# Kernel tuning notes

Hardware: AMD Instinct MI355X
Metric: run time of the kernel (lower is better)

The kernel has to match this reference:

```python
import jax, jax.numpy as jnp
from jax import lax
import numpy as np

B, L, D = 8, 2048, 512
Q, K = 8, 2048


def setup_inputs() -> dict:
    key = jax.random.key(0)
    kx, kc = jax.random.split(key)
    x = jax.random.normal(kx, (B, L, D), dtype=jnp.float32)
    codebooks = jax.random.normal(kc, (Q, K, D), dtype=jnp.float32)  # Q stacked [K, D] embedding tables
    return {"x": x, "codebooks": codebooks}


def reference(x, codebooks):
    # Residual VQ: at each level, nearest-codeword lookup on the residual.
    # cdist argmin == squared-distance argmin: ||r||^2 - 2 r.c + ||c||^2.
    cb_sq = jnp.sum(codebooks * codebooks, axis=-1)  # [Q, K]

    def step(residual, level):
        cb, cb2 = level  # [K, D], [K]
        r2 = jnp.sum(residual * residual, axis=-1, keepdims=True)  # [B, L, 1]
        dots = jnp.einsum('bld,kd->blk', residual, cb)  # [B, L, K]
        dist2 = r2 - 2.0 * dots + cb2  # [B, L, K]
        idx = jnp.argmin(dist2, axis=-1)  # [B, L]
        quant = cb[idx]  # [B, L, D] gather
        return residual - quant, (idx, quant)

    _, (indices, quants) = lax.scan(step, x, (codebooks, cb_sq))
    quantized = jnp.sum(quants, axis=0)  # [B, L, D]
    indices = jnp.moveaxis(indices, 0, 1)  # [B, Q, L] (torch.stack(dim=1))
    return indices, quantized
```

## Files before the change

### kernel.cpp

```cpp
#include <hip/hip_runtime.h>

#define BB 8
#define LL 2048
#define DD 512
#define QQ 8
#define KK 2048
#define MM (BB*LL)

#define NTILES 16

typedef __attribute__((ext_vector_type(8))) short short8;
typedef __attribute__((ext_vector_type(4))) float f32x4;

#define GLDS(src, dst) __builtin_amdgcn_global_load_lds( \
    (const __attribute__((address_space(1))) void*)(src), \
    (__attribute__((address_space(3))) void*)(dst), 16, 0, 0)

#define BARX()  asm volatile("s_barrier" ::: "memory")
#define WAIT0() asm volatile("s_waitcnt vmcnt(0)" ::: "memory")

__device__ __forceinline__ ushort f2bf(float f) {
    uint u = __float_as_uint(f);
    u += 0x7FFFu + ((u >> 16) & 1u);
    return (ushort)(u >> 16);
}

__global__ __launch_bounds__(256) void cb2_kernel(const float* __restrict__ cb,
                                                  float* __restrict__ cb2) {
    int row  = blockIdx.x * 4 + (threadIdx.x >> 6);
    int lane = threadIdx.x & 63;
    const float* r = cb + (size_t)row * DD + lane * 8;
    float4 a = *(const float4*)r;
    float4 b = *(const float4*)(r + 4);
    float s = a.x*a.x + a.y*a.y + a.z*a.z + a.w*a.w
            + b.x*b.x + b.y*b.y + b.z*b.z + b.w*b.w;
    #pragma unroll
    for (int off = 32; off >= 1; off >>= 1) s += __shfl_xor(s, off);
    if (lane == 0) cb2[row] = s;
}

__global__ __launch_bounds__(256) void bprep_kernel(const float* __restrict__ cbq,
                                                    short8* __restrict__ bh2) {
    const int wid  = threadIdx.x >> 6;
    const int lane = threadIdx.x & 63;
    const int col  = blockIdx.x * 4 + wid;
    const float* src = cbq + (size_t)col * DD + lane * 8;
    float4 v0 = *(const float4*)src;
    float4 v1 = *(const float4*)(src + 4);
    short8 h;
    h[0] = (short)f2bf(v0.x); h[1] = (short)f2bf(v0.y);
    h[2] = (short)f2bf(v0.z); h[3] = (short)f2bf(v0.w);
    h[4] = (short)f2bf(v1.x); h[5] = (short)f2bf(v1.y);
    h[6] = (short)f2bf(v1.z); h[7] = (short)f2bf(v1.w);
    bh2[(size_t)col * 64 + lane] = h;
}

__global__ __launch_bounds__(256) void aprep0_kernel(const float* __restrict__ x,
                                                     float* __restrict__ resid,
                                                     short8* __restrict__ ah) {
    const int wid  = threadIdx.x >> 6;
    const int lane = threadIdx.x & 63;
    const int row  = blockIdx.x * 4 + wid;
    const float* src = x + (size_t)row * DD + lane * 8;
    float4 v0 = *(const float4*)src;
    float4 v1 = *(const float4*)(src + 4);
    float* dst = resid + (size_t)row * DD + lane * 8;
    *(float4*)dst       = v0;
    *(float4*)(dst + 4) = v1;
    short8 h;
    h[0] = (short)f2bf(v0.x); h[1] = (short)f2bf(v0.y);
    h[2] = (short)f2bf(v0.z); h[3] = (short)f2bf(v0.w);
    h[4] = (short)f2bf(v1.x); h[5] = (short)f2bf(v1.y);
    h[6] = (short)f2bf(v1.z); h[7] = (short)f2bf(v1.w);
    ah[(size_t)row * 64 + lane] = h;
}

__global__ __launch_bounds__(512, 2) void gemm_argmin_kernel(
    const short8* __restrict__ ah,
    const short8* __restrict__ bh2,
    const float*  __restrict__ cb2q,
    float*        __restrict__ blockv1,
    uint4*        __restrict__ blockmask,
    float W)
{
    __shared__ char smemc[131072];

    const int id  = blockIdx.x;
    const int xcd = id & 7;
    const int s   = id >> 3;
    const int nt  = s & 7;
    const int mt  = xcd * 8 + (s >> 3);

    const int tid  = threadIdx.x;
    const int wid  = tid >> 6;
    const int lane = tid & 63;
    const int wr   = wid >> 2;
    const int wcn  = wid & 3;
    const int l15  = lane & 15, l4 = lane >> 4;

    f32x4 acc[4][8];
    #pragma unroll
    for (int n = 0; n < 4; n++)
        #pragma unroll
        for (int m = 0; m < 8; m++) acc[n][m] = (f32x4){0.f, 0.f, 0.f, 0.f};

    const char* aSrc = (const char*)ah  + ((size_t)mt << 18);
    const char* bSrc = (const char*)bh2 + ((size_t)nt << 18);

    #define STAGEQ(tt, bufn, p) do { \
        int g_ = (p) * 512 + tid; \
        int rL_ = g_ >> 3, st_ = g_ & 7; \
        int k_ = st_ ^ (rL_ & 7); \
        char* db_ = smemc + (bufn) * 65536 + ((p) * 512 + wid * 64) * 16; \
        GLDS(aSrc + (size_t)rL_ * 1024 + (tt) * 128 + k_ * 16, db_); \
        GLDS(bSrc + (size_t)rL_ * 1024 + (tt) * 128 + k_ * 16, db_ + 32768); \
    } while (0)

    short8 af[4][2], bf[4][2];

    #define LDA(mh) do { \
        _Pragma("unroll") for (int mm = 0; mm < 4; mm++) \
        _Pragma("unroll") for (int ks = 0; ks < 2; ks++) { \
            int rL_ = wr * 128 + ((mh) * 4 + mm) * 16 + l15; \
            int c_ = ks * 4 + l4; \
            af[mm][ks] = *(const short8*)(smemc + ab + rL_ * 128 + ((c_ ^ (rL_ & 7)) << 4)); \
        } } while (0)

    #define LDB(nh) do { \
        _Pragma("unroll") for (int nn = 0; nn < 2; nn++) \
        _Pragma("unroll") for (int ks = 0; ks < 2; ks++) { \
            int cL_ = wcn * 64 + ((nh) * 2 + nn) * 16 + l15; \
            int c_ = ks * 4 + l4; \
            bf[(nh)*2+nn][ks] = *(const short8*)(smemc + ab + 32768 + cL_ * 128 + ((c_ ^ (cL_ & 7)) << 4)); \
        } } while (0)

    #define PH(mh, nh) do { \
        __builtin_amdgcn_s_setprio(1); \
        _Pragma("unroll") for (int nn = 0; nn < 2; nn++) \
        _Pragma("unroll") for (int mm = 0; mm < 4; mm++) \
        _Pragma("unroll") for (int ks = 0; ks < 2; ks++) \
            acc[(nh)*2+nn][(mh)*4+mm] = __builtin_amdgcn_mfma_f32_16x16x32_bf16( \
                bf[(nh)*2+nn][ks], af[mm][ks], acc[(nh)*2+nn][(mh)*4+mm], 0, 0, 0); \
        __builtin_amdgcn_s_setprio(0); \
    } while (0)

    STAGEQ(0, 0, 0); STAGEQ(0, 0, 1); STAGEQ(0, 0, 2); STAGEQ(0, 0, 3);
    WAIT0();
    BARX();

    for (int t = 0; t < 8; t++) {
        const uint ab = (uint)(t & 1) * 65536u;
        const int nbuf = (t & 1) ^ 1;
        LDA(0); LDB(0);
        if (t < 7) { STAGEQ(t + 1, nbuf, 0); STAGEQ(t + 1, nbuf, 1); }
        PH(0, 0);
        BARX();
        LDB(1);
        if (t < 7) { STAGEQ(t + 1, nbuf, 2); STAGEQ(t + 1, nbuf, 3); }
        PH(0, 1);
        BARX();
        LDA(1);
        PH(1, 0);
        BARX();
        PH(1, 1);
        if (t < 7) WAIT0();
        BARX();
    }

    float* halfmin = (float*)smemc;
    uint2* maskS   = (uint2*)(smemc + 4096);

    f32x4 c2v[4];
    #pragma unroll
    for (int n = 0; n < 4; n++)
        c2v[n] = *(const f32x4*)&cb2q[nt * 256 + wcn * 64 + n * 16 + (l4 << 2)];

    #pragma unroll
    for (int m = 0; m < 8; m++) {
        float v = 3.4e38f;
        #pragma unroll
        for (int n = 0; n < 4; n++)
            #pragma unroll
            for (int r = 0; r < 4; r++)
                v = fminf(v, fmaf(-2.f, acc[n][m][r], c2v[n][r]));
        v = fminf(v, __shfl_xor(v, 16));
        v = fminf(v, __shfl_xor(v, 32));
        if (l4 == 0) halfmin[(wr * 128 + m * 16 + l15) * 4 + wcn] = v;
    }
    __syncthreads();

    #pragma unroll
    for (int m = 0; m < 8; m++) {
        int rL = wr * 128 + m * 16 + l15;
        int pb = wcn & 2;
        float vt = fminf(halfmin[rL * 4 + pb], halfmin[rL * 4 + pb + 1]);
        float thrm = vt + W;
        uint blo = 0, bhi = 0;
        #pragma unroll
        for (int n = 0; n < 4; n++)
            #pragma unroll
            for (int r = 0; r < 4; r++) {
                float d = fmaf(-2.f, acc[n][m][r], c2v[n][r]);
                int bit = n * 16 + (l4 << 2) + r;
                if (d < thrm) { if (bit < 32) blo |= 1u << bit; else bhi |= 1u << (bit - 32); }
            }
        blo |= __shfl_xor(blo, 16); bhi |= __shfl_xor(bhi, 16);
        blo |= __shfl_xor(blo, 32); bhi |= __shfl_xor(bhi, 32);
        if (l4 == 0) maskS[rL * 4 + wcn] = make_uint2(blo, bhi);
    }
    __syncthreads();

    {
        int T = tid >> 8, rL = tid & 255;
        float vt = fminf(halfmin[rL * 4 + T * 2], halfmin[rL * 4 + T * 2 + 1]);
        uint2 lo = maskS[rL * 4 + T * 2], hi = maskS[rL * 4 + T * 2 + 1];
        size_t o = (size_t)(nt * 2 + T) * MM + mt * 256 + rL;
        blockv1[o] = vt;
        blockmask[o] = make_uint4(lo.x, lo.y, hi.x, hi.y);
    }
    #undef STAGEQ
    #undef LDA
    #undef LDB
    #undef PH
}

__global__ __launch_bounds__(256) void crru_kernel(
    const float*  __restrict__ blockv1,
    const uint4*  __restrict__ blockmask,
    const float*  __restrict__ cbq,
    const float*  __restrict__ cb2q,
    float*        __restrict__ resid,
    float*        __restrict__ idx_out,
    short8*       __restrict__ ah,
    int q, float W)
{
    __shared__ float rs[4][DD];
    const int wid  = threadIdx.x >> 6;
    const int lane = threadIdx.x & 63;
    const int row  = blockIdx.x * 4 + wid;
    const int grp  = lane >> 4, gl = lane & 15;

    float v1 = 3.4e38f;
    uint4 mk = make_uint4(0, 0, 0, 0);
    if (lane < NTILES) {
        size_t o = (size_t)lane * MM + row;
        v1 = blockv1[o];
        mk = blockmask[o];
    }

    float* rrow = resid + (size_t)row * DD + lane * 8;
    float4 r0 = *(const float4*)rrow;
    float4 r1 = *(const float4*)(rrow + 4);
    *(float4*)&rs[wid][lane * 8]     = r0;
    *(float4*)&rs[wid][lane * 8 + 4] = r1;

    float g1 = v1;
    #pragma unroll
    for (int off = 32; off >= 1; off >>= 1) g1 = fminf(g1, __shfl_xor(g1, off));
    const float thr = g1 + W;

    unsigned long long act = __ballot((lane < NTILES) && (v1 < thr));

    float be = 3.4e38f; int bk = 0x7FFFFFFF;
    const float* rsw = rs[wid];

    auto eval4 = [&](int k0, int k1, int k2, int k3) {
        int kg = (grp == 0) ? k0 : (grp == 1) ? k1 : (grp == 2) ? k2 : k3;
        float d = 0.f;
        if (kg >= 0) {
            const float* cp = cbq + (size_t)kg * DD + gl * 32;
            const float* rp = rsw + gl * 32;
            #pragma unroll
            for (int j = 0; j < 8; j++) {
                float4 c = *(const float4*)(cp + j * 4);
                float4 r = *(const float4*)(rp + j * 4);
                d = fmaf(r.x, c.x, d); d = fmaf(r.y, c.y, d);
                d = fmaf(r.z, c.z, d); d = fmaf(r.w, c.w, d);
            }
        }
        #pragma unroll
        for (int off = 8; off >= 1; off >>= 1) d += __shfl_xor(d, off);
        #pragma unroll
        for (int g = 0; g < 4; g++) {
            float dg = __shfl(d, g * 16);
            int kg2 = (g == 0) ? k0 : (g == 1) ? k1 : (g == 2) ? k2 : k3;
            if (kg2 >= 0) {
                float e = fmaf(-2.f, dg, cb2q[kg2]);
                if (e < be || (e == be && kg2 < bk)) { be = e; bk = kg2; }
            }
        }
    };

    while (act) {
        int tile = __ffsll(act) - 1; act &= act - 1;
        uint m0 = __shfl((int)mk.x, tile), m1 = __shfl((int)mk.y, tile);
        uint m2 = __shfl((int)mk.z, tile), m3 = __shfl((int)mk.w, tile);
        unsigned long long lo = ((unsigned long long)m1 << 32) | m0;
        unsigned long long hi = ((unsigned long long)m3 << 32) | m2;
        int base = tile * 128;
        while (lo | hi) {
            int c0 = -1, c1 = -1, c2 = -1, c3 = -1;
            #define POP1(dst) \
                if (lo) { int b = __ffsll(lo) - 1; lo &= lo - 1; dst = base + b; } \
                else if (hi) { int b = __ffsll(hi) - 1; hi &= hi - 1; dst = base + 64 + b; }
            POP1(c0) POP1(c1) POP1(c2) POP1(c3)
            #undef POP1
            eval4(c0, c1, c2, c3);
        }
    }
    const int winner = bk;

    if (lane == 0) {
        int b = row >> 11, l = row & (LL - 1);
        idx_out[((size_t)b * QQ + q) * LL + l] = (float)winner;
    }

    const float* cw = cbq + (size_t)winner * DD + lane * 8;
    float4 c0 = *(const float4*)cw;
    float4 c1 = *(const float4*)(cw + 4);
    float4 n0 = make_float4(r0.x - c0.x, r0.y - c0.y, r0.z - c0.z, r0.w - c0.w);
    float4 n1 = make_float4(r1.x - c1.x, r1.y - c1.y, r1.z - c1.z, r1.w - c1.w);
    *(float4*)rrow       = n0;
    *(float4*)(rrow + 4) = n1;

    if (q < QQ - 1) {
        short8 h;
        h[0] = (short)f2bf(n0.x); h[1] = (short)f2bf(n0.y);
        h[2] = (short)f2bf(n0.z); h[3] = (short)f2bf(n0.w);
        h[4] = (short)f2bf(n1.x); h[5] = (short)f2bf(n1.y);
        h[6] = (short)f2bf(n1.z); h[7] = (short)f2bf(n1.w);
        ah[(size_t)row * 64 + lane] = h;
    }
}

__global__ __launch_bounds__(256) void final_kernel(const float* __restrict__ x,
                                                    float* __restrict__ qout) {
    size_t i = (size_t)blockIdx.x * 256 + threadIdx.x;
    float4 xv = ((const float4*)x)[i];
    float4 rv = ((float4*)qout)[i];
    ((float4*)qout)[i] = make_float4(xv.x - rv.x, xv.y - rv.y, xv.z - rv.z, xv.w - rv.w);
}

extern "C" void kernel_launch(void* const* d_in, const int* in_sizes, int n_in,
                              void* d_out, int out_size, void* d_ws, size_t ws_size,
                              hipStream_t stream) {
    (void)in_sizes; (void)n_in; (void)out_size; (void)ws_size;
    const float* x  = (const float*)d_in[0];
    const float* cb = (const float*)d_in[1];
    float* out = (float*)d_out;

    float* idx_out = out;
    float* resid   = out + (size_t)BB * QQ * LL;

    char* w = (char*)d_ws;
    float*  cb2       = (float*)(w);
    float*  blockv1   = (float*)(w + 0x10000);
    uint4*  blockmask = (uint4*)(w + 0x110000);
    short8* ah        = (short8*)(w + 0x510000);
    short8* bh2       = (short8*)(w + 0x1510000);

    cb2_kernel<<<QQ * KK / 4, 256, 0, stream>>>(cb, cb2);
    aprep0_kernel<<<MM / 4, 256, 0, stream>>>(x, resid, ah);

    for (int q = 0; q < QQ; q++) {
        const float* cbq = cb + (size_t)q * KK * DD;
        const float* c2q = cb2 + (size_t)q * KK;
        const float W = 2.0f + 0.3f * q;

        bprep_kernel<<<KK / 4, 256, 0, stream>>>(cbq, bh2);

        gemm_argmin_kernel<<<512, 512, 0, stream>>>(ah, bh2, c2q,
                                                    blockv1, blockmask, W);

        crru_kernel<<<MM / 4, 256, 0, stream>>>(blockv1, blockmask, cbq, c2q, resid,
                                                idx_out, ah, q, W);
    }

    final_kernel<<<MM * DD / 4 / 256, 256, 0, stream>>>(x, resid);
}
```

Baseline: 523.4 us.

## Simplify GEMM k-loop to one barrier per tile and fuse final subtraction

```diff
diff --git a/kernel.cpp b/kernel.cpp
--- a/kernel.cpp
+++ b/kernel.cpp
@@ -126,21 +126,21 @@
             af[mm][ks] = *(const short8*)(smemc + ab + rL_ * 128 + ((c_ ^ (rL_ & 7)) << 4)); \
         } } while (0)
 
-    #define LDB(nh) do { \
-        _Pragma("unroll") for (int nn = 0; nn < 2; nn++) \
+    #define LDBALL() do { \
+        _Pragma("unroll") for (int nn = 0; nn < 4; nn++) \
         _Pragma("unroll") for (int ks = 0; ks < 2; ks++) { \
-            int cL_ = wcn * 64 + ((nh) * 2 + nn) * 16 + l15; \
+            int cL_ = wcn * 64 + nn * 16 + l15; \
             int c_ = ks * 4 + l4; \
-            bf[(nh)*2+nn][ks] = *(const short8*)(smemc + ab + 32768 + cL_ * 128 + ((c_ ^ (cL_ & 7)) << 4)); \
+            bf[nn][ks] = *(const short8*)(smemc + ab + 32768 + cL_ * 128 + ((c_ ^ (cL_ & 7)) << 4)); \
         } } while (0)
 
-    #define PH(mh, nh) do { \
+    #define PH(mh) do { \
         __builtin_amdgcn_s_setprio(1); \
-        _Pragma("unroll") for (int nn = 0; nn < 2; nn++) \
+        _Pragma("unroll") for (int ks = 0; ks < 2; ks++) \
+        _Pragma("unroll") for (int nn = 0; nn < 4; nn++) \
         _Pragma("unroll") for (int mm = 0; mm < 4; mm++) \
-        _Pragma("unroll") for (int ks = 0; ks < 2; ks++) \
-            acc[(nh)*2+nn][(mh)*4+mm] = __builtin_amdgcn_mfma_f32_16x16x32_bf16( \
-                bf[(nh)*2+nn][ks], af[mm][ks], acc[(nh)*2+nn][(mh)*4+mm], 0, 0, 0); \
+            acc[nn][(mh)*4+mm] = __builtin_amdgcn_mfma_f32_16x16x32_bf16( \
+                bf[nn][ks], af[mm][ks], acc[nn][(mh)*4+mm], 0, 0, 0); \
         __builtin_amdgcn_s_setprio(0); \
     } while (0)
 
@@ -151,18 +151,13 @@
     for (int t = 0; t < 8; t++) {
         const uint ab = (uint)(t & 1) * 65536u;
         const int nbuf = (t & 1) ^ 1;
-        LDA(0); LDB(0);
-        if (t < 7) { STAGEQ(t + 1, nbuf, 0); STAGEQ(t + 1, nbuf, 1); }
-        PH(0, 0);
-        BARX();
-        LDB(1);
-        if (t < 7) { STAGEQ(t + 1, nbuf, 2); STAGEQ(t + 1, nbuf, 3); }
-        PH(0, 1);
-        BARX();
+        if (t < 7) { STAGEQ(t + 1, nbuf, 0); STAGEQ(t + 1, nbuf, 1);
+                     STAGEQ(t + 1, nbuf, 2); STAGEQ(t + 1, nbuf, 3); }
+        LDBALL();
+        LDA(0);
+        PH(0);
         LDA(1);
-        PH(1, 0);
-        BARX();
-        PH(1, 1);
+        PH(1);
         if (t < 7) WAIT0();
         BARX();
     }
@@ -220,7 +215,7 @@
     }
     #undef STAGEQ
     #undef LDA
-    #undef LDB
+    #undef LDBALL
     #undef PH
 }
 
@@ -229,6 +224,7 @@
     const uint4*  __restrict__ blockmask,
     const float*  __restrict__ cbq,
     const float*  __restrict__ cb2q,
+    const float*  __restrict__ xin,
     float*        __restrict__ resid,
     float*        __restrict__ idx_out,
     short8*       __restrict__ ah,
@@ -320,25 +316,23 @@
     float4 c1 = *(const float4*)(cw + 4);
     float4 n0 = make_float4(r0.x - c0.x, r0.y - c0.y, r0.z - c0.z, r0.w - c0.w);
     float4 n1 = make_float4(r1.x - c1.x, r1.y - c1.y, r1.z - c1.z, r1.w - c1.w);
-    *(float4*)rrow       = n0;
-    *(float4*)(rrow + 4) = n1;
 
     if (q < QQ - 1) {
+        *(float4*)rrow       = n0;
+        *(float4*)(rrow + 4) = n1;
         short8 h;
         h[0] = (short)f2bf(n0.x); h[1] = (short)f2bf(n0.y);
         h[2] = (short)f2bf(n0.z); h[3] = (short)f2bf(n0.w);
         h[4] = (short)f2bf(n1.x); h[5] = (short)f2bf(n1.y);
         h[6] = (short)f2bf(n1.z); h[7] = (short)f2bf(n1.w);
         ah[(size_t)row * 64 + lane] = h;
-    }
-}
-
-__global__ __launch_bounds__(256) void final_kernel(const float* __restrict__ x,
-                                                    float* __restrict__ qout) {
-    size_t i = (size_t)blockIdx.x * 256 + threadIdx.x;
-    float4 xv = ((const float4*)x)[i];
-    float4 rv = ((float4*)qout)[i];
-    ((float4*)qout)[i] = make_float4(xv.x - rv.x, xv.y - rv.y, xv.z - rv.z, xv.w - rv.w);
+    } else {
+        const float* xw = xin + (size_t)row * DD + lane * 8;
+        float4 x0 = *(const float4*)xw;
+        float4 x1 = *(const float4*)(xw + 4);
+        *(float4*)rrow       = make_float4(x0.x - n0.x, x0.y - n0.y, x0.z - n0.z, x0.w - n0.w);
+        *(float4*)(rrow + 4) = make_float4(x1.x - n1.x, x1.y - n1.y, x1.z - n1.z, x1.w - n1.w);
+    }
 }
 
 extern "C" void kernel_launch(void* const* d_in, const int* in_sizes, int n_in,
@@ -372,9 +366,7 @@
         gemm_argmin_kernel<<<512, 512, 0, stream>>>(ah, bh2, c2q,
                                                     blockv1, blockmask, W);
 
-        crru_kernel<<<MM / 4, 256, 0, stream>>>(blockv1, blockmask, cbq, c2q, resid,
-                                                idx_out, ah, q, W);
-    }
-
-    final_kernel<<<MM * DD / 4 / 256, 256, 0, stream>>>(x, resid);
-}
+        crru_kernel<<<MM / 4, 256, 0, stream>>>(blockv1, blockmask, cbq, c2q, x,
+                                                resid, idx_out, ah, q, W);
+    }
+}
```

Measured after the change: 517.1 us. About the same (-1.2%).
